# Kernel tuning notes

Measured on AMD Instinct MI355X. Metric: run time of the kernel, lower is better.

The kernel has to match this reference:

```python
import jax, jax.numpy as jnp
import numpy as np

IN_FEATURES = 4096
OUT_FEATURES = 12288


def setup_inputs() -> dict:
    key = jax.random.key(0)
    k1, k2, k3 = jax.random.split(key, 3)
    inp = jax.random.normal(k1, (2, 2048, IN_FEATURES), dtype=jnp.float32)
    # int8 quantized weight, [out_features, in_features]
    quant_w = jax.random.randint(k2, (OUT_FEATURES, IN_FEATURES), -128, 128, dtype=jnp.int32).astype(jnp.int8)
    # per-output-channel scale, small positive (typical ~ max|w|/127)
    scale_w = (jax.random.uniform(k3, (OUT_FEATURES,), dtype=jnp.float32) + 0.5) * 0.02
    return {"inp": inp, "quant_w": quant_w, "scale_w": scale_w}


def reference(inp, quant_w, scale_w):
    # extract_weight_to_half: dequantize int8 weight with per-channel scale
    weight = quant_w.astype(inp.dtype) * scale_w[:, None]        # [N, K]
    # inp.view(-1, K) @ weight.T, reshaped back -> fuse via einsum
    out = jnp.einsum("bsk,nk->bsn", inp, weight)                 # [B, S, N]
    return out
```

## Files before the change

kernel.cpp:

```cpp
#include <hip/hip_runtime.h>
#include <hip/hip_bf16.h>


#define K_DIM 4096
#define N_DIM 12288

constexpr int BM = 256;
constexpr int BN = 256;
constexpr int BKB = 128;
constexpr int NT = K_DIM / BKB;

typedef float  f32x4  __attribute__((ext_vector_type(4)));
typedef int    i32x4  __attribute__((ext_vector_type(4)));
typedef short  bf16x8 __attribute__((ext_vector_type(8)));
typedef unsigned short u16x4 __attribute__((ext_vector_type(4)));

__device__ __forceinline__ unsigned short f32_to_bf16(float f) {
    unsigned int u = __builtin_bit_cast(unsigned int, f);
    u += 0x7FFFu + ((u >> 16) & 1u);
    return (unsigned short)(u >> 16);
}


__global__ __launch_bounds__(256)
void quant_a_kernel(const float* __restrict__ A,
                    signed char* __restrict__ Aq,
                    float* __restrict__ Ra) {
    const int row  = blockIdx.x;
    const int tid  = threadIdx.x;
    const int lane = tid & 63;
    const int wid  = tid >> 6;
    const float* arow = A + (size_t)row * K_DIM;
    const int base = tid * 16;

    f32x4 v[4];
    #pragma unroll
    for (int i = 0; i < 4; ++i)
        v[i] = *(const f32x4*)(arow + base + i * 4);

    float mx = 0.f;
    #pragma unroll
    for (int i = 0; i < 4; ++i)
        #pragma unroll
        for (int j = 0; j < 4; ++j)
            mx = fmaxf(mx, fabsf(v[i][j]));

    #pragma unroll
    for (int off = 32; off > 0; off >>= 1)
        mx = fmaxf(mx, __shfl_xor(mx, off));

    __shared__ float wmax[4];
    if (lane == 0) wmax[wid] = mx;
    __syncthreads();
    mx = fmaxf(fmaxf(wmax[0], wmax[1]), fmaxf(wmax[2], wmax[3]));

    const float inv = (mx > 0.f) ? (127.0f / mx) : 0.f;
    if (tid == 0) Ra[row] = mx * (1.0f / 127.0f);

    int p[4];
    #pragma unroll
    for (int i = 0; i < 4; ++i) {
        int b0 = (int)rintf(v[i][0] * inv);
        int b1 = (int)rintf(v[i][1] * inv);
        int b2 = (int)rintf(v[i][2] * inv);
        int b3 = (int)rintf(v[i][3] * inv);
        p[i] = (b0 & 255) | ((b1 & 255) << 8) | ((b2 & 255) << 16) | (b3 << 24);
    }
    *(i32x4*)(Aq + (size_t)row * K_DIM + base) = *(i32x4*)p;
}


__global__ __launch_bounds__(256)
void pack_w_kernel(const int* __restrict__ W, signed char* __restrict__ Wpk, int nchunk) {
    int stride = gridDim.x * blockDim.x;
    for (int gid = blockIdx.x * blockDim.x + threadIdx.x; gid < nchunk; gid += stride) {
        const int l   = gid & 63;
        const int blk = gid >> 6;
        const int ks  = blk & 1;
        const int g   = (blk >> 1) & 15;
        const int kt  = (blk >> 5) & 31;
        const int B   = blk >> 10;
        const int n   = B * 256 + (g >> 2) * 64 + (g & 3) * 16 + (l & 15);
        const int kb  = kt * 128 + ks * 64 + ((l >> 4) * 16);
        const int* src = W + (size_t)n * K_DIM + kb;
        int p[4];
        #pragma unroll
        for (int q = 0; q < 4; ++q) {
            const i32x4 w = *(const i32x4*)(src + q * 4);
            p[q] = (w[0] & 255) | ((w[1] & 255) << 8) | ((w[2] & 255) << 16) | (w[3] << 24);
        }
        *(i32x4*)(Wpk + (size_t)gid * 16) = *(i32x4*)p;
    }
}


__device__ __forceinline__ void gload_lds16(const void* g, void* l) {
    __builtin_amdgcn_global_load_lds(
        (const __attribute__((address_space(1))) unsigned int*)g,
        (__attribute__((address_space(3))) unsigned int*)l,
        16, 0, 0);
}

__global__ __launch_bounds__(512, 2)
void gemm_i8_256(const signed char* __restrict__ Aq,
                 const signed char* __restrict__ Wpk,
                 const float* __restrict__ Sw,
                 const float* __restrict__ Ra,
                 float* __restrict__ Out,
                 int M) {
    __shared__ __align__(16) unsigned char As8[2][BM * BKB];

    const int tid  = threadIdx.x;
    const int lane = tid & 63;
    const int wid  = tid >> 6;
    const int wm   = wid >> 2;
    const int wn   = wid & 3;

    const int nwgy = M / BM;
    const int nwg  = (N_DIM / BN) * nwgy;
    const int cpx  = nwg >> 3;
    const int bid  = blockIdx.x;
    const int swz  = (bid & 7) * cpx + (bid >> 3);
    const int bx   = swz / nwgy;
    const int by   = swz % nwgy;
    const int bm   = by * BM;
    const int bn   = bx * BN;

    const int srow  = wid * 8 + (lane >> 3);
    const int scolB = ((lane & 7) ^ (lane >> 3)) * 16;

    #define STG_A(k0B, L)                                                            \
        do {                                                                         \
            gload_lds16(Aq + (size_t)(bm + srow) * K_DIM + (k0B) + scolB,            \
                        (L) + wid * 1024);                                           \
            gload_lds16(Aq + (size_t)(bm + 64 + srow) * K_DIM + (k0B) + scolB,       \
                        (L) + 8192 + wid * 1024);                                    \
            gload_lds16(Aq + (size_t)(bm + 128 + srow) * K_DIM + (k0B) + scolB,      \
                        (L) + 16384 + wid * 1024);                                   \
            gload_lds16(Aq + (size_t)(bm + 192 + srow) * K_DIM + (k0B) + scolB,      \
                        (L) + 24576 + wid * 1024);                                   \
        } while (0)

    i32x4 acc[8][4];
    #pragma unroll
    for (int i = 0; i < 8; ++i)
        #pragma unroll
        for (int j = 0; j < 4; ++j)
            acc[i][j] = (i32x4){0, 0, 0, 0};

    const int c0   = lane & 15;
    const int kgB  = (lane >> 4) * 16;
    const int rswB = (c0 & 7) * 16;

    i32x4 af[8][2];
    i32x4 bf0[2][2];
    i32x4 bf1[2][2];

    const int aoffA = (wm * 128 + c0) * BKB;

    const signed char* Wbase = Wpk + ((size_t)((bn >> 8) * 32) << 10) * 32 + lane * 16;

    #define LD_B(dst, kt, q0)                                                        \
        _Pragma("unroll") for (int nf = 0; nf < 2; ++nf)                            \
        _Pragma("unroll") for (int ks = 0; ks < 2; ++ks)                            \
            (dst)[nf][ks] = *(const i32x4*)(Wbase +                                  \
                ((size_t)((kt) * 32 + (wn * 4 + (q0) + nf) * 2 + (ks)) << 10));

    #define RD_A(base, BUF, row0)                                                   \
        _Pragma("unroll") for (int mf = 0; mf < 4; ++mf)                            \
        _Pragma("unroll") for (int ks = 0; ks < 2; ++ks)                            \
            af[(base) + mf][ks] = *(const i32x4*)&As8[BUF][aoffA + ((row0) + mf * 16) * BKB + ((ks * 64 + kgB) ^ rswB)];

    #define CLUSTER(qm, qn, BF)                                                     \
        _Pragma("unroll") for (int ks = 0; ks < 2; ++ks)                            \
        _Pragma("unroll") for (int mf = 0; mf < 4; ++mf)                            \
        _Pragma("unroll") for (int nf = 0; nf < 2; ++nf)                            \
            acc[(qm)*4 + mf][(qn)*2 + nf] = __builtin_amdgcn_mfma_i32_16x16x64_i8(  \
                af[(qm)*4 + mf][ks], (BF)[nf][ks], acc[(qm)*4 + mf][(qn)*2 + nf],   \
                0, 0, 0);

    STG_A(0, &As8[0][0]);
    LD_B(bf0, 0, 0);
    STG_A(BKB, &As8[1][0]);
    LD_B(bf1, 0, 2);
    asm volatile("s_waitcnt vmcnt(8)" ::: "memory");
    __builtin_amdgcn_s_barrier();

    for (int t = 0; t < NT; ++t) {
        const int cur = t & 1;
        const int kt1 = (t + 1 < NT) ? (t + 1) : (NT - 1);
        const int kt2 = (t + 2 < NT) ? (t + 2) : (NT - 1);

        RD_A(0, cur, 0);
        RD_A(4, cur, 64);
        __builtin_amdgcn_s_barrier();
        asm volatile("s_waitcnt lgkmcnt(0)");
        asm volatile("s_waitcnt vmcnt(8)" ::: "memory");
        __builtin_amdgcn_s_setprio(1);
        CLUSTER(0, 0, bf0);
        CLUSTER(1, 0, bf0);
        __builtin_amdgcn_s_setprio(0);

        LD_B(bf0, kt1, 0);
        STG_A(kt2 * BKB, &As8[cur][0]);
        asm volatile("s_waitcnt vmcnt(8)" ::: "memory");
        __builtin_amdgcn_s_setprio(1);
        CLUSTER(0, 1, bf1);
        CLUSTER(1, 1, bf1);
        __builtin_amdgcn_s_setprio(0);
        LD_B(bf1, kt1, 2);
        __builtin_amdgcn_s_barrier();
    }
    #undef CLUSTER
    #undef RD_A
    #undef LD_B
    #undef STG_A

    const int r0 = (lane >> 4) * 4;
    float rav[8][4];
    #pragma unroll
    for (int m = 0; m < 8; ++m)
        #pragma unroll
        for (int j = 0; j < 4; ++j)
            rav[m][j] = Ra[bm + wm * 128 + m * 16 + r0 + j];

    #pragma unroll
    for (int n = 0; n < 4; ++n) {
        const int col = bn + wn * 64 + n * 16 + c0;
        const float s = Sw[col];
        #pragma unroll
        for (int m = 0; m < 8; ++m) {
            const int rowb = bm + wm * 128 + m * 16 + r0;
            #pragma unroll
            for (int j = 0; j < 4; ++j)
                Out[(size_t)(rowb + j) * N_DIM + col] = (float)acc[m][n][j] * s * rav[m][j];
        }
    }
}


constexpr int FBM = 128, FBN = 128, FBK = 64, FPAD = 8;

__global__ __launch_bounds__(256)
void qlinear_fused_kernel(const float* __restrict__ A, const int* __restrict__ Wqi,
                          const float* __restrict__ Sw, float* __restrict__ Out, int M) {
    __shared__ unsigned short Asf[FBM][FBK + FPAD];
    __shared__ unsigned short Bsf[FBN][FBK + FPAD];
    const int tid  = threadIdx.x;
    const int lane = tid & 63;
    const int wid  = tid >> 6;
    const int wm   = wid >> 1;
    const int wn   = wid & 1;
    const int bm = blockIdx.y * FBM;
    const int bn = blockIdx.x * FBN;
    const int rowT = tid >> 4;
    const int kq   = tid & 15;
    f32x4 acc[4][4];
    #pragma unroll
    for (int i = 0; i < 4; ++i)
        #pragma unroll
        for (int j = 0; j < 4; ++j) acc[i][j] = (f32x4){0.f,0.f,0.f,0.f};
    const int c0 = lane & 15;
    const int kg = (lane >> 4) * 8;
    for (int k0 = 0; k0 < K_DIM; k0 += FBK) {
        #pragma unroll
        for (int it = 0; it < 8; ++it) {
            const int r = it * 16 + rowT;
            const f32x4 a4 = *(const f32x4*)(A + (size_t)(bm + r) * K_DIM + k0 + kq * 4);
            u16x4 h;
            h[0]=f32_to_bf16(a4[0]); h[1]=f32_to_bf16(a4[1]);
            h[2]=f32_to_bf16(a4[2]); h[3]=f32_to_bf16(a4[3]);
            *(u16x4*)&Asf[r][kq*4] = h;
        }
        #pragma unroll
        for (int it = 0; it < 8; ++it) {
            const int r = it * 16 + rowT;
            const i32x4 w4 = *(const i32x4*)(Wqi + (size_t)(bn + r) * K_DIM + k0 + kq * 4);
            u16x4 h;
            h[0]=f32_to_bf16((float)w4[0]); h[1]=f32_to_bf16((float)w4[1]);
            h[2]=f32_to_bf16((float)w4[2]); h[3]=f32_to_bf16((float)w4[3]);
            *(u16x4*)&Bsf[r][kq*4] = h;
        }
        __syncthreads();
        #pragma unroll
        for (int ks = 0; ks < 2; ++ks) {
            const int kk = ks * 32 + kg;
            bf16x8 af2[4], bfr[4];
            #pragma unroll
            for (int mf = 0; mf < 4; ++mf)
                af2[mf] = *(const bf16x8*)&Asf[wm*64 + mf*16 + c0][kk];
            #pragma unroll
            for (int nf = 0; nf < 4; ++nf)
                bfr[nf] = *(const bf16x8*)&Bsf[wn*64 + nf*16 + c0][kk];
            #pragma unroll
            for (int mf = 0; mf < 4; ++mf)
                #pragma unroll
                for (int nf = 0; nf < 4; ++nf)
                    acc[mf][nf] = __builtin_amdgcn_mfma_f32_16x16x32_bf16(
                        af2[mf], bfr[nf], acc[mf][nf], 0, 0, 0);
        }
        __syncthreads();
    }
    const int r0 = (lane >> 4) * 4;
    #pragma unroll
    for (int nf = 0; nf < 4; ++nf) {
        const int col = bn + wn*64 + nf*16 + c0;
        const float s = Sw[col];
        #pragma unroll
        for (int mf = 0; mf < 4; ++mf) {
            const int rowb = bm + wm*64 + mf*16 + r0;
            #pragma unroll
            for (int j = 0; j < 4; ++j)
                Out[(size_t)(rowb + j) * N_DIM + col] = acc[mf][nf][j] * s;
        }
    }
}

extern "C" void kernel_launch(void* const* d_in, const int* in_sizes, int n_in,
                              void* d_out, int out_size, void* d_ws, size_t ws_size,
                              hipStream_t stream) {
    const float* inp = (const float*)d_in[0];
    const int*   qw  = (const int*)d_in[1];
    const float* sw  = (const float*)d_in[2];
    float*       out = (float*)d_out;

    const int M = in_sizes[0] / K_DIM;
    const size_t nA = (size_t)M * K_DIM;
    const size_t nW = (size_t)N_DIM * K_DIM;
    const size_t needQ = nA + nW + (size_t)M * sizeof(float);

    if (ws_size >= needQ && (M % BM) == 0) {
        signed char* Aq  = (signed char*)d_ws;
        signed char* Wpk = Aq + nA;
        float*       Ra  = (float*)(Wpk + nW);
        quant_a_kernel<<<M, 256, 0, stream>>>(inp, Aq, Ra);
        pack_w_kernel<<<2048, 256, 0, stream>>>(qw, Wpk, (int)(nW / 16));
        dim3 grid((N_DIM / BN) * (M / BM));
        gemm_i8_256<<<grid, 512, 0, stream>>>(Aq, Wpk, sw, Ra, out, M);
    } else {
        dim3 grid(N_DIM / FBN, M / FBM);
        qlinear_fused_kernel<<<grid, 256, 0, stream>>>(inp, qw, sw, out, M);
    }
}
```

Before: 319.6 us.

## Replace LDS-staged int8 GEMM with direct register loads from pre-packed A and W

The activation quantization kernel now writes A directly into an MFMA-fragment-packed layout, and the weight packing is changed to a simple per-16-column layout. The GEMM drops shared memory entirely: each wave loads its A and B fragments straight from global memory into registers, with a 128x128 tile and higher occupancy. This removes LDS staging, barriers and swizzling. In exchange there is no data reuse across waves through LDS, so global/L2 traffic per FLOP rises sharply, and the software pipelining of loads is gone.

```diff
diff --git a/kernel.cpp b/kernel.cpp
--- a/kernel.cpp
+++ b/kernel.cpp
@@ -5,10 +5,9 @@
 #define K_DIM 4096
 #define N_DIM 12288
 
-constexpr int BM = 256;
-constexpr int BN = 256;
-constexpr int BKB = 128;
-constexpr int NT = K_DIM / BKB;
+constexpr int BM = 128;
+constexpr int BN = 128;
+constexpr int NT = K_DIM / 128;
 
 typedef float  f32x4  __attribute__((ext_vector_type(4)));
 typedef int    i32x4  __attribute__((ext_vector_type(4)));
@@ -23,9 +22,9 @@
 
 
 __global__ __launch_bounds__(256)
-void quant_a_kernel(const float* __restrict__ A,
-                    signed char* __restrict__ Aq,
-                    float* __restrict__ Ra) {
+void quant_a_pack(const float* __restrict__ A,
+                  signed char* __restrict__ Apk,
+                  float* __restrict__ Ra) {
     const int row  = blockIdx.x;
     const int tid  = threadIdx.x;
     const int lane = tid & 63;
@@ -66,7 +65,16 @@
         int b3 = (int)rintf(v[i][3] * inv);
         p[i] = (b0 & 255) | ((b1 & 255) << 8) | ((b2 & 255) << 16) | (b3 << 24);
     }
-    *(i32x4*)(Aq + (size_t)row * K_DIM + base) = *(i32x4*)p;
+
+    const int k16  = tid;
+    const int kt   = k16 >> 3;
+    const int ks   = (k16 >> 2) & 1;
+    const int hi   = k16 & 3;
+    const int ln   = hi * 16 + (row & 15);
+    const int mf   = (row >> 4) & 3;
+    const int r64  = row >> 6;
+    const size_t off = (((((size_t)r64 * 32 + kt) * 4 + mf) * 2 + ks) << 10) + ln * 16;
+    *(i32x4*)(Apk + off) = *(i32x4*)p;
 }
 
 
@@ -77,10 +85,9 @@
         const int l   = gid & 63;
         const int blk = gid >> 6;
         const int ks  = blk & 1;
-        const int g   = (blk >> 1) & 15;
-        const int kt  = (blk >> 5) & 31;
-        const int B   = blk >> 10;
-        const int n   = B * 256 + (g >> 2) * 64 + (g & 3) * 16 + (l & 15);
+        const int kt  = (blk >> 1) & 31;
+        const int n16 = blk >> 6;
+        const int n   = n16 * 16 + (l & 15);
         const int kb  = kt * 128 + ks * 64 + ((l >> 4) * 16);
         const int* src = W + (size_t)n * K_DIM + kb;
         int p[4];
@@ -94,22 +101,13 @@
 }
 
 
-__device__ __forceinline__ void gload_lds16(const void* g, void* l) {
-    __builtin_amdgcn_global_load_lds(
-        (const __attribute__((address_space(1))) unsigned int*)g,
-        (__attribute__((address_space(3))) unsigned int*)l,
-        16, 0, 0);
-}
-
-__global__ __launch_bounds__(512, 2)
-void gemm_i8_256(const signed char* __restrict__ Aq,
-                 const signed char* __restrict__ Wpk,
-                 const float* __restrict__ Sw,
-                 const float* __restrict__ Ra,
-                 float* __restrict__ Out,
-                 int M) {
-    __shared__ __align__(16) unsigned char As8[2][BM * BKB];
-
+__global__ __launch_bounds__(512, 4)
+void gemm_i8_nolds(const signed char* __restrict__ Apk,
+                   const signed char* __restrict__ Wpk,
+                   const float* __restrict__ Sw,
+                   const float* __restrict__ Ra,
+                   float* __restrict__ Out,
+                   int M) {
     const int tid  = threadIdx.x;
     const int lane = tid & 63;
     const int wid  = tid >> 6;
@@ -126,114 +124,57 @@
     const int bm   = by * BM;
     const int bn   = bx * BN;
 
-    const int srow  = wid * 8 + (lane >> 3);
-    const int scolB = ((lane & 7) ^ (lane >> 3)) * 16;
-
-    #define STG_A(k0B, L)                                                            \
-        do {                                                                         \
-            gload_lds16(Aq + (size_t)(bm + srow) * K_DIM + (k0B) + scolB,            \
-                        (L) + wid * 1024);                                           \
-            gload_lds16(Aq + (size_t)(bm + 64 + srow) * K_DIM + (k0B) + scolB,       \
-                        (L) + 8192 + wid * 1024);                                    \
-            gload_lds16(Aq + (size_t)(bm + 128 + srow) * K_DIM + (k0B) + scolB,      \
-                        (L) + 16384 + wid * 1024);                                   \
-            gload_lds16(Aq + (size_t)(bm + 192 + srow) * K_DIM + (k0B) + scolB,      \
-                        (L) + 24576 + wid * 1024);                                   \
-        } while (0)
-
-    i32x4 acc[8][4];
-    #pragma unroll
-    for (int i = 0; i < 8; ++i)
-        #pragma unroll
-        for (int j = 0; j < 4; ++j)
+    const int r64     = by * 2 + wm;
+    const int n16base = bx * 8 + wn * 2;
+
+    const signed char* Ab = Apk + (((size_t)r64) << 18) + lane * 16;
+    const signed char* Bb = Wpk + (((size_t)n16base) << 16) + lane * 16;
+
+    i32x4 acc[4][2];
+    #pragma unroll
+    for (int i = 0; i < 4; ++i)
+        #pragma unroll
+        for (int j = 0; j < 2; ++j)
             acc[i][j] = (i32x4){0, 0, 0, 0};
 
-    const int c0   = lane & 15;
-    const int kgB  = (lane >> 4) * 16;
-    const int rswB = (c0 & 7) * 16;
-
-    i32x4 af[8][2];
-    i32x4 bf0[2][2];
-    i32x4 bf1[2][2];
-
-    const int aoffA = (wm * 128 + c0) * BKB;
-
-    const signed char* Wbase = Wpk + ((size_t)((bn >> 8) * 32) << 10) * 32 + lane * 16;
-
-    #define LD_B(dst, kt, q0)                                                        \
-        _Pragma("unroll") for (int nf = 0; nf < 2; ++nf)                            \
-        _Pragma("unroll") for (int ks = 0; ks < 2; ++ks)                            \
-            (dst)[nf][ks] = *(const i32x4*)(Wbase +                                  \
-                ((size_t)((kt) * 32 + (wn * 4 + (q0) + nf) * 2 + (ks)) << 10));
-
-    #define RD_A(base, BUF, row0)                                                   \
-        _Pragma("unroll") for (int mf = 0; mf < 4; ++mf)                            \
-        _Pragma("unroll") for (int ks = 0; ks < 2; ++ks)                            \
-            af[(base) + mf][ks] = *(const i32x4*)&As8[BUF][aoffA + ((row0) + mf * 16) * BKB + ((ks * 64 + kgB) ^ rswB)];
-
-    #define CLUSTER(qm, qn, BF)                                                     \
-        _Pragma("unroll") for (int ks = 0; ks < 2; ++ks)                            \
-        _Pragma("unroll") for (int mf = 0; mf < 4; ++mf)                            \
-        _Pragma("unroll") for (int nf = 0; nf < 2; ++nf)                            \
-            acc[(qm)*4 + mf][(qn)*2 + nf] = __builtin_amdgcn_mfma_i32_16x16x64_i8(  \
-                af[(qm)*4 + mf][ks], (BF)[nf][ks], acc[(qm)*4 + mf][(qn)*2 + nf],   \
-                0, 0, 0);
-
-    STG_A(0, &As8[0][0]);
-    LD_B(bf0, 0, 0);
-    STG_A(BKB, &As8[1][0]);
-    LD_B(bf1, 0, 2);
-    asm volatile("s_waitcnt vmcnt(8)" ::: "memory");
-    __builtin_amdgcn_s_barrier();
-
-    for (int t = 0; t < NT; ++t) {
-        const int cur = t & 1;
-        const int kt1 = (t + 1 < NT) ? (t + 1) : (NT - 1);
-        const int kt2 = (t + 2 < NT) ? (t + 2) : (NT - 1);
-
-        RD_A(0, cur, 0);
-        RD_A(4, cur, 64);
-        __builtin_amdgcn_s_barrier();
-        asm volatile("s_waitcnt lgkmcnt(0)");
-        asm volatile("s_waitcnt vmcnt(8)" ::: "memory");
+    for (int kt = 0; kt < NT; ++kt) {
+        i32x4 af[4][2];
+        i32x4 bf[2][2];
+        #pragma unroll
+        for (int mf = 0; mf < 4; ++mf)
+            #pragma unroll
+            for (int ks = 0; ks < 2; ++ks)
+                af[mf][ks] = *(const i32x4*)(Ab + (((size_t)(kt * 8 + mf * 2 + ks)) << 10));
+        #pragma unroll
+        for (int nf = 0; nf < 2; ++nf)
+            #pragma unroll
+            for (int ks = 0; ks < 2; ++ks)
+                bf[nf][ks] = *(const i32x4*)(Bb + (((size_t)(nf * 64 + kt * 2 + ks)) << 10));
+
         __builtin_amdgcn_s_setprio(1);
-        CLUSTER(0, 0, bf0);
-        CLUSTER(1, 0, bf0);
+        #pragma unroll
+        for (int ks = 0; ks < 2; ++ks)
+            #pragma unroll
+            for (int mf = 0; mf < 4; ++mf)
+                #pragma unroll
+                for (int nf = 0; nf < 2; ++nf)
+                    acc[mf][nf] = __builtin_amdgcn_mfma_i32_16x16x64_i8(
+                        af[mf][ks], bf[nf][ks], acc[mf][nf], 0, 0, 0);
         __builtin_amdgcn_s_setprio(0);
-
-        LD_B(bf0, kt1, 0);
-        STG_A(kt2 * BKB, &As8[cur][0]);
-        asm volatile("s_waitcnt vmcnt(8)" ::: "memory");
-        __builtin_amdgcn_s_setprio(1);
-        CLUSTER(0, 1, bf1);
-        CLUSTER(1, 1, bf1);
-        __builtin_amdgcn_s_setprio(0);
-        LD_B(bf1, kt1, 2);
-        __builtin_amdgcn_s_barrier();
-    }
-    #undef CLUSTER
-    #undef RD_A
-    #undef LD_B
-    #undef STG_A
-
+    }
+
+    const int c0 = lane & 15;
     const int r0 = (lane >> 4) * 4;
-    float rav[8][4];
-    #pragma unroll
-    for (int m = 0; m < 8; ++m)
-        #pragma unroll
-        for (int j = 0; j < 4; ++j)
-            rav[m][j] = Ra[bm + wm * 128 + m * 16 + r0 + j];
-
-    #pragma unroll
-    for (int n = 0; n < 4; ++n) {
-        const int col = bn + wn * 64 + n * 16 + c0;
+    #pragma unroll
+    for (int nf = 0; nf < 2; ++nf) {
+        const int col = bn + wn * 32 + nf * 16 + c0;
         const float s = Sw[col];
         #pragma unroll
-        for (int m = 0; m < 8; ++m) {
-            const int rowb = bm + wm * 128 + m * 16 + r0;
+        for (int mf = 0; mf < 4; ++mf) {
+            const int rowb = bm + wm * 64 + mf * 16 + r0;
             #pragma unroll
             for (int j = 0; j < 4; ++j)
-                Out[(size_t)(rowb + j) * N_DIM + col] = (float)acc[m][n][j] * s * rav[m][j];
+                Out[(size_t)(rowb + j) * N_DIM + col] = (float)acc[mf][nf][j] * s * Ra[rowb + j];
         }
     }
 }
@@ -330,13 +271,13 @@
     const size_t needQ = nA + nW + (size_t)M * sizeof(float);
 
     if (ws_size >= needQ && (M % BM) == 0) {
-        signed char* Aq  = (signed char*)d_ws;
-        signed char* Wpk = Aq + nA;
+        signed char* Apk = (signed char*)d_ws;
+        signed char* Wpk = Apk + nA;
         float*       Ra  = (float*)(Wpk + nW);
-        quant_a_kernel<<<M, 256, 0, stream>>>(inp, Aq, Ra);
+        quant_a_pack<<<M, 256, 0, stream>>>(inp, Apk, Ra);
         pack_w_kernel<<<2048, 256, 0, stream>>>(qw, Wpk, (int)(nW / 16));
         dim3 grid((N_DIM / BN) * (M / BM));
-        gemm_i8_256<<<grid, 512, 0, stream>>>(Aq, Wpk, sw, Ra, out, M);
+        gemm_i8_nolds<<<grid, 512, 0, stream>>>(Apk, Wpk, sw, Ra, out, M);
     } else {
         dim3 grid(N_DIM / FBN, M / FBM);
         qlinear_fused_kernel<<<grid, 256, 0, stream>>>(inp, qw, sw, out, M);
```

New measurement: 447.3 us, median of 4. 1.4x slower.
